# Optimization experiments

Measured on AMD Instinct MI355X. Metric: run time of the kernel, lower is better.

## Reference

```python
import jax, jax.numpy as jnp
import numpy as np

NEG_SLOPE = 0.2


def _add_self_loops(edge_index, n_nodes):
    loop = jnp.arange(n_nodes, dtype=edge_index.dtype)
    src = jnp.concatenate([edge_index[0], loop])
    dst = jnp.concatenate([edge_index[1], loop])
    return src, dst


def _gat_layer(x, src, dst, W, a_src, a_dst, b):
    # PyG GATConv, heads=1: h = x @ W; e_ij = LeakyReLU(a_src.h_j + a_dst.h_i)
    # softmax over incoming edges of each dst node, then weighted aggregate.
    n = x.shape[0]
    h = x @ W                      # [N, d]
    s = h @ a_src                  # [N] per-source score
    t = h @ a_dst                  # [N] per-dest score
    e = jax.nn.leaky_relu(s[src] + t[dst], NEG_SLOPE)          # [E]
    m = jax.ops.segment_max(e, dst, num_segments=n)            # stable softmax
    ex = jnp.exp(e - m[dst])
    denom = jax.ops.segment_sum(ex, dst, num_segments=n)
    alpha = ex / denom[dst]                                     # [E]
    out = jax.ops.segment_sum(h[src] * alpha[:, None], dst, num_segments=n)
    return out + b


def setup_inputs() -> dict:
    key = jax.random.key(0)
    ks = jax.random.split(key, 16)
    N, E, d = 50000, 800000, 64
    sc = 1.0 / np.sqrt(d)
    inp = {
        "x": jax.random.normal(ks[0], (N, d), dtype=jnp.float32),
        "edge_index": jax.random.randint(ks[1], (2, E), 0, N, dtype=jnp.int64),
    }
    for i, layer in enumerate((1, 2, 3)):
        inp[f"W{layer}"] = jax.random.normal(ks[2 + 4 * i], (d, d), dtype=jnp.float32) * sc
        inp[f"a_src{layer}"] = jax.random.normal(ks[3 + 4 * i], (d,), dtype=jnp.float32) * sc
        inp[f"a_dst{layer}"] = jax.random.normal(ks[4 + 4 * i], (d,), dtype=jnp.float32) * sc
        inp[f"b{layer}"] = jnp.zeros((d,), dtype=jnp.float32)
    return inp


def reference(x, edge_index, W1, a_src1, a_dst1, b1, W2, a_src2, a_dst2, b2,
              W3, a_src3, a_dst3, b3):
    n = x.shape[0]
    src, dst = _add_self_loops(edge_index, n)
    x = jax.nn.relu(_gat_layer(x, src, dst, W1, a_src1, a_dst1, b1))
    x = jax.nn.relu(_gat_layer(x, src, dst, W2, a_src2, a_dst2, b2))
    x = jax.nn.relu(_gat_layer(x, src, dst, W3, a_src3, a_dst3, b3))
    return x
```

## Files before the change

kernel.cpp:

```cpp
#include <hip/hip_runtime.h>
#include <hip/hip_fp16.h>

#define NEG_SLOPE 0.2f
#define MAXDEG 64

__device__ __forceinline__ float readlane_f(float v, int l) {
    return __uint_as_float(__builtin_amdgcn_readlane(__float_as_uint(v), l));
}
__device__ __forceinline__ int readlane_i(int v, int l) {
    return __builtin_amdgcn_readlane(v, l);
}


__device__ __forceinline__ void bucket_body(const int* __restrict__ ei, int E,
                                            int* __restrict__ cnt, int* __restrict__ slots,
                                            int bid) {
    int t = bid * 256 + threadIdx.x;
    int base = t * 8;
    if (base >= E) return;
    int s[8], d[8];
    if (base + 7 < E) {
        int4 sa = *(const int4*)(ei + base);
        int4 sb = *(const int4*)(ei + base + 4);
        int4 da = *(const int4*)(ei + E + base);
        int4 db = *(const int4*)(ei + E + base + 4);
        s[0]=sa.x; s[1]=sa.y; s[2]=sa.z; s[3]=sa.w; s[4]=sb.x; s[5]=sb.y; s[6]=sb.z; s[7]=sb.w;
        d[0]=da.x; d[1]=da.y; d[2]=da.z; d[3]=da.w; d[4]=db.x; d[5]=db.y; d[6]=db.z; d[7]=db.w;
    } else {
        #pragma unroll
        for (int j = 0; j < 8; j++) {
            int e = base + j;
            if (e < E) { s[j] = ei[e]; d[j] = ei[E + e]; }
            else       { s[j] = -1;    d[j] = -1; }
        }
    }
    int pos[8];
    #pragma unroll
    for (int j = 0; j < 8; j++)
        pos[j] = (d[j] >= 0) ? atomicAdd(&cnt[d[j]], 1) : MAXDEG;
    #pragma unroll
    for (int j = 0; j < 8; j++)
        if (pos[j] < MAXDEG)
            __builtin_nontemporal_store(s[j], &slots[(size_t)d[j] * MAXDEG + pos[j]]);
}


__device__ __forceinline__ void gemm_body(const float* __restrict__ x, const float* __restrict__ W,
                                          const float* __restrict__ a_src, const float* __restrict__ a_dst,
                                          __half* __restrict__ h16, float* __restrict__ sv,
                                          float* __restrict__ tv, int n, int bid) {
    __shared__ float Wl[64 * 64];
    __shared__ float Xl[64 * 68];
    int tid = threadIdx.x;
    int n0 = bid * 64;

    #pragma unroll
    for (int r = 0; r < 4; r++) {
        int f = tid + r * 256;
        int k = f >> 4, c = (f & 15) * 4;
        *(float4*)(&Wl[k * 64 + c]) = *(const float4*)(W + (size_t)f * 4);
    }
    #pragma unroll
    for (int r = 0; r < 4; r++) {
        int f = tid + r * 256;
        int node = f >> 4, k = (f & 15) * 4;
        float4 xv = make_float4(0.f, 0.f, 0.f, 0.f);
        if (n0 + node < n) xv = *(const float4*)(x + (size_t)(n0 + node) * 64 + k);
        Xl[(k + 0) * 68 + node] = xv.x;
        Xl[(k + 1) * 68 + node] = xv.y;
        Xl[(k + 2) * 68 + node] = xv.z;
        Xl[(k + 3) * 68 + node] = xv.w;
    }
    __syncthreads();

    int tx = tid & 15, ty = tid >> 4;
    float acc[4][4] = {{0.f}};
    #pragma unroll 16
    for (int k = 0; k < 64; k++) {
        float4 xv = *(const float4*)(&Xl[k * 68 + ty * 4]);
        float4 wv = *(const float4*)(&Wl[k * 64 + tx * 4]);
        acc[0][0] += xv.x * wv.x; acc[0][1] += xv.x * wv.y; acc[0][2] += xv.x * wv.z; acc[0][3] += xv.x * wv.w;
        acc[1][0] += xv.y * wv.x; acc[1][1] += xv.y * wv.y; acc[1][2] += xv.y * wv.z; acc[1][3] += xv.y * wv.w;
        acc[2][0] += xv.z * wv.x; acc[2][1] += xv.z * wv.y; acc[2][2] += xv.z * wv.z; acc[2][3] += xv.z * wv.w;
        acc[3][0] += xv.w * wv.x; acc[3][1] += xv.w * wv.y; acc[3][2] += xv.w * wv.z; acc[3][3] += xv.w * wv.w;
    }

    float4 as4 = *(const float4*)(a_src + tx * 4);
    float4 ad4 = *(const float4*)(a_dst + tx * 4);
    #pragma unroll
    for (int j = 0; j < 4; j++) {
        int node = n0 + ty * 4 + j;
        float sp = acc[j][0] * as4.x + acc[j][1] * as4.y + acc[j][2] * as4.z + acc[j][3] * as4.w;
        float tp = acc[j][0] * ad4.x + acc[j][1] * ad4.y + acc[j][2] * ad4.z + acc[j][3] * ad4.w;
        #pragma unroll
        for (int o = 1; o < 16; o <<= 1) {
            sp += __shfl_xor(sp, o);
            tp += __shfl_xor(tp, o);
        }
        if (node < n) {
            union { __half2 h2[2]; uint2 u; } pk;
            pk.h2[0] = __floats2half2_rn(acc[j][0], acc[j][1]);
            pk.h2[1] = __floats2half2_rn(acc[j][2], acc[j][3]);
            *(uint2*)(h16 + (size_t)node * 64 + tx * 4) = pk.u;
            if (tx == 0) { sv[node] = sp; tv[node] = tp; }
        }
    }
}

__global__ __launch_bounds__(256) void k_fused1(const int* __restrict__ ei, int E,
                                                int* __restrict__ cnt, int* __restrict__ slots,
                                                const float* __restrict__ x, const float* __restrict__ W,
                                                const float* __restrict__ a_src, const float* __restrict__ a_dst,
                                                __half* __restrict__ h16, float* __restrict__ sv,
                                                float* __restrict__ tv, int n, int gB) {
    int bid = blockIdx.x;
    if (bid < gB) bucket_body(ei, E, cnt, slots, bid);
    else          gemm_body(x, W, a_src, a_dst, h16, sv, tv, n, bid - gB);
}

__global__ __launch_bounds__(256) void k_gemm(const float* __restrict__ x, const float* __restrict__ W,
                                              const float* __restrict__ a_src, const float* __restrict__ a_dst,
                                              __half* __restrict__ h16, float* __restrict__ sv,
                                              float* __restrict__ tv, int n) {
    gemm_body(x, W, a_src, a_dst, h16, sv, tv, n, blockIdx.x);
}


#define GATHER8(K)                                                            \
    {                                                                         \
        float e0 = readlane_f(ex, (K) + 0), e1 = readlane_f(ex, (K) + 1);     \
        float e2 = readlane_f(ex, (K) + 2), e3 = readlane_f(ex, (K) + 3);     \
        float e4 = readlane_f(ex, (K) + 4), e5 = readlane_f(ex, (K) + 5);     \
        float e6 = readlane_f(ex, (K) + 6), e7 = readlane_f(ex, (K) + 7);     \
        int s0 = readlane_i(sid, (K) + 0), s1 = readlane_i(sid, (K) + 1);     \
        int s2 = readlane_i(sid, (K) + 2), s3 = readlane_i(sid, (K) + 3);     \
        int s4 = readlane_i(sid, (K) + 4), s5 = readlane_i(sid, (K) + 5);     \
        int s6 = readlane_i(sid, (K) + 6), s7 = readlane_i(sid, (K) + 7);     \
        float v0 = __half2float(h16[(size_t)s0 * 64 + lane]);                 \
        float v1 = __half2float(h16[(size_t)s1 * 64 + lane]);                 \
        float v2 = __half2float(h16[(size_t)s2 * 64 + lane]);                 \
        float v3 = __half2float(h16[(size_t)s3 * 64 + lane]);                 \
        float v4 = __half2float(h16[(size_t)s4 * 64 + lane]);                 \
        float v5 = __half2float(h16[(size_t)s5 * 64 + lane]);                 \
        float v6 = __half2float(h16[(size_t)s6 * 64 + lane]);                 \
        float v7 = __half2float(h16[(size_t)s7 * 64 + lane]);                 \
        acc0 += e0 * v0; acc1 += e1 * v1; acc2 += e2 * v2; acc3 += e3 * v3;   \
        acc0 += e4 * v4; acc1 += e5 * v5; acc2 += e6 * v6; acc3 += e7 * v7;   \
    }

__global__ __launch_bounds__(1024) void k_agg(const __half* __restrict__ h16, const float* __restrict__ sv,
                                              const float* __restrict__ tv, const int* __restrict__ cnt,
                                              const int* __restrict__ slots, const float* __restrict__ bias,
                                              float* __restrict__ xout, int n) {
    int wid = (blockIdx.x * 1024 + threadIdx.x) >> 6;
    int lane = threadIdx.x & 63;
    if (wid >= n) return;
    int deg = cnt[wid];
    if (deg > 63) deg = 63;
    int ecount = deg + 1;
    float tn = tv[wid];

    int sid = 0;
    bool valid = lane < ecount;
    if (valid) sid = (lane == deg) ? wid : slots[(size_t)wid * MAXDEG + lane];
    float ss = valid ? sv[sid] : 0.f;
    float ev = ss + tn;
    ev = (ev > 0.f) ? ev : NEG_SLOPE * ev;
    float ex = valid ? __expf(ev) : 0.f;

    float denom = ex;
    #pragma unroll
    for (int o = 1; o < 64; o <<= 1) denom += __shfl_xor(denom, o);

    float acc0 = 0.f, acc1 = 0.f, acc2 = 0.f, acc3 = 0.f;
    if (ecount <= 24) {
        GATHER8(0) GATHER8(8) GATHER8(16)
    } else {
        int cnt8 = (ecount + 7) & ~7;
        for (int k = 0; k < cnt8; k += 8) GATHER8(k)
    }

    float o = (acc0 + acc1) + (acc2 + acc3);
    o = o / denom + bias[lane];
    xout[(size_t)wid * 64 + lane] = fmaxf(o, 0.f);
}


extern "C" void kernel_launch(void* const* d_in, const int* in_sizes, int n_in,
                              void* d_out, int out_size, void* d_ws, size_t ws_size,
                              hipStream_t stream) {
    const float* x0 = (const float*)d_in[0];
    const int* ei = (const int*)d_in[1];
    const float* Wp[3]    = {(const float*)d_in[2],  (const float*)d_in[6],  (const float*)d_in[10]};
    const float* asp[3]   = {(const float*)d_in[3],  (const float*)d_in[7],  (const float*)d_in[11]};
    const float* adp[3]   = {(const float*)d_in[4],  (const float*)d_in[8],  (const float*)d_in[12]};
    const float* bp[3]    = {(const float*)d_in[5],  (const float*)d_in[9],  (const float*)d_in[13]};

    int N = in_sizes[0] / 64;
    int E = in_sizes[1] / 2;

    size_t nf = (size_t)N * 64;
    float* bufA = (float*)d_ws;
    float* sArr = bufA + nf;
    float* tArr = sArr + N;
    int* cntArr = (int*)(tArr + N);
    int* slots  = cntArr + N;
    __half* h16 = (__half*)(slots + (size_t)N * MAXDEG);

    hipMemsetAsync(cntArr, 0, (size_t)N * sizeof(int), stream);

    int gB = ((E + 7) / 8 + 255) / 256;
    int gG = (N + 63) / 64;
    int gAgg = (N + 15) / 16;

    k_fused1<<<gB + gG, 256, 0, stream>>>(ei, E, cntArr, slots,
                                          x0, Wp[0], asp[0], adp[0], h16, sArr, tArr, N, gB);
    k_agg<<<gAgg, 1024, 0, stream>>>(h16, sArr, tArr, cntArr, slots, bp[0], bufA, N);
    k_gemm<<<gG, 256, 0, stream>>>(bufA, Wp[1], asp[1], adp[1], h16, sArr, tArr, N);
    k_agg<<<gAgg, 1024, 0, stream>>>(h16, sArr, tArr, cntArr, slots, bp[1], bufA, N);
    k_gemm<<<gG, 256, 0, stream>>>(bufA, Wp[2], asp[2], adp[2], h16, sArr, tArr, N);
    k_agg<<<gAgg, 1024, 0, stream>>>(h16, sArr, tArr, cntArr, slots, bp[2], (float*)d_out, N);
}
```

Before: 181.7 us.

## Fuse aggregation with next layer's GEMM via shared-memory tile

Adds a k_fusedA kernel in which each 256-thread block aggregates 64 destination nodes (16 per wave) and writes the ReLU'd results into shared memory. It then runs the next layer's 64x64 GEMM and attention-score dots on that tile directly, double-buffering h16/s/t across layers. This removes the fp32 intermediate round trip through global memory and two kernel launches. In exchange, the aggregation runs with fewer threads per block and the blocks process their nodes serially, which may lower the parallelism available to hide gather latency.

```diff
diff --git a/kernel.cpp b/kernel.cpp
--- a/kernel.cpp
+++ b/kernel.cpp
@@ -45,34 +45,11 @@
 }
 
 
-__device__ __forceinline__ void gemm_body(const float* __restrict__ x, const float* __restrict__ W,
-                                          const float* __restrict__ a_src, const float* __restrict__ a_dst,
-                                          __half* __restrict__ h16, float* __restrict__ sv,
-                                          float* __restrict__ tv, int n, int bid) {
-    __shared__ float Wl[64 * 64];
-    __shared__ float Xl[64 * 68];
+__device__ __forceinline__ void gemm_compute(const float* __restrict__ Wl, const float* __restrict__ Xl,
+                                             const float* __restrict__ a_src, const float* __restrict__ a_dst,
+                                             __half* __restrict__ h16, float* __restrict__ sv,
+                                             float* __restrict__ tv, int n, int n0) {
     int tid = threadIdx.x;
-    int n0 = bid * 64;
-
-    #pragma unroll
-    for (int r = 0; r < 4; r++) {
-        int f = tid + r * 256;
-        int k = f >> 4, c = (f & 15) * 4;
-        *(float4*)(&Wl[k * 64 + c]) = *(const float4*)(W + (size_t)f * 4);
-    }
-    #pragma unroll
-    for (int r = 0; r < 4; r++) {
-        int f = tid + r * 256;
-        int node = f >> 4, k = (f & 15) * 4;
-        float4 xv = make_float4(0.f, 0.f, 0.f, 0.f);
-        if (n0 + node < n) xv = *(const float4*)(x + (size_t)(n0 + node) * 64 + k);
-        Xl[(k + 0) * 68 + node] = xv.x;
-        Xl[(k + 1) * 68 + node] = xv.y;
-        Xl[(k + 2) * 68 + node] = xv.z;
-        Xl[(k + 3) * 68 + node] = xv.w;
-    }
-    __syncthreads();
-
     int tx = tid & 15, ty = tid >> 4;
     float acc[4][4] = {{0.f}};
     #pragma unroll 16
@@ -84,7 +61,6 @@
         acc[2][0] += xv.z * wv.x; acc[2][1] += xv.z * wv.y; acc[2][2] += xv.z * wv.z; acc[2][3] += xv.z * wv.w;
         acc[3][0] += xv.w * wv.x; acc[3][1] += xv.w * wv.y; acc[3][2] += xv.w * wv.z; acc[3][3] += xv.w * wv.w;
     }
-
     float4 as4 = *(const float4*)(a_src + tx * 4);
     float4 ad4 = *(const float4*)(a_dst + tx * 4);
     #pragma unroll
@@ -107,6 +83,36 @@
     }
 }
 
+
+__device__ __forceinline__ void gemm_body(const float* __restrict__ x, const float* __restrict__ W,
+                                          const float* __restrict__ a_src, const float* __restrict__ a_dst,
+                                          __half* __restrict__ h16, float* __restrict__ sv,
+                                          float* __restrict__ tv, int n, int bid) {
+    __shared__ float Wl[64 * 64];
+    __shared__ float Xl[64 * 68];
+    int tid = threadIdx.x;
+    int n0 = bid * 64;
+    #pragma unroll
+    for (int r = 0; r < 4; r++) {
+        int f = tid + r * 256;
+        int k = f >> 4, c = (f & 15) * 4;
+        *(float4*)(&Wl[k * 64 + c]) = *(const float4*)(W + (size_t)f * 4);
+    }
+    #pragma unroll
+    for (int r = 0; r < 4; r++) {
+        int f = tid + r * 256;
+        int node = f >> 4, k = (f & 15) * 4;
+        float4 xv = make_float4(0.f, 0.f, 0.f, 0.f);
+        if (n0 + node < n) xv = *(const float4*)(x + (size_t)(n0 + node) * 64 + k);
+        Xl[(k + 0) * 68 + node] = xv.x;
+        Xl[(k + 1) * 68 + node] = xv.y;
+        Xl[(k + 2) * 68 + node] = xv.z;
+        Xl[(k + 3) * 68 + node] = xv.w;
+    }
+    __syncthreads();
+    gemm_compute(Wl, Xl, a_src, a_dst, h16, sv, tv, n, n0);
+}
+
 __global__ __launch_bounds__(256) void k_fused1(const int* __restrict__ ei, int E,
                                                 int* __restrict__ cnt, int* __restrict__ slots,
                                                 const float* __restrict__ x, const float* __restrict__ W,
@@ -118,15 +124,8 @@
     else          gemm_body(x, W, a_src, a_dst, h16, sv, tv, n, bid - gB);
 }
 
-__global__ __launch_bounds__(256) void k_gemm(const float* __restrict__ x, const float* __restrict__ W,
-                                              const float* __restrict__ a_src, const float* __restrict__ a_dst,
-                                              __half* __restrict__ h16, float* __restrict__ sv,
-                                              float* __restrict__ tv, int n) {
-    gemm_body(x, W, a_src, a_dst, h16, sv, tv, n, blockIdx.x);
-}
-
-
-#define GATHER8(K)                                                            \
+
+#define GATHER8(H, K)                                                         \
     {                                                                         \
         float e0 = readlane_f(ex, (K) + 0), e1 = readlane_f(ex, (K) + 1);     \
         float e2 = readlane_f(ex, (K) + 2), e3 = readlane_f(ex, (K) + 3);     \
@@ -136,17 +135,75 @@
         int s2 = readlane_i(sid, (K) + 2), s3 = readlane_i(sid, (K) + 3);     \
         int s4 = readlane_i(sid, (K) + 4), s5 = readlane_i(sid, (K) + 5);     \
         int s6 = readlane_i(sid, (K) + 6), s7 = readlane_i(sid, (K) + 7);     \
-        float v0 = __half2float(h16[(size_t)s0 * 64 + lane]);                 \
-        float v1 = __half2float(h16[(size_t)s1 * 64 + lane]);                 \
-        float v2 = __half2float(h16[(size_t)s2 * 64 + lane]);                 \
-        float v3 = __half2float(h16[(size_t)s3 * 64 + lane]);                 \
-        float v4 = __half2float(h16[(size_t)s4 * 64 + lane]);                 \
-        float v5 = __half2float(h16[(size_t)s5 * 64 + lane]);                 \
-        float v6 = __half2float(h16[(size_t)s6 * 64 + lane]);                 \
-        float v7 = __half2float(h16[(size_t)s7 * 64 + lane]);                 \
+        float v0 = __half2float(H[(size_t)s0 * 64 + lane]);                   \
+        float v1 = __half2float(H[(size_t)s1 * 64 + lane]);                   \
+        float v2 = __half2float(H[(size_t)s2 * 64 + lane]);                   \
+        float v3 = __half2float(H[(size_t)s3 * 64 + lane]);                   \
+        float v4 = __half2float(H[(size_t)s4 * 64 + lane]);                   \
+        float v5 = __half2float(H[(size_t)s5 * 64 + lane]);                   \
+        float v6 = __half2float(H[(size_t)s6 * 64 + lane]);                   \
+        float v7 = __half2float(H[(size_t)s7 * 64 + lane]);                   \
         acc0 += e0 * v0; acc1 += e1 * v1; acc2 += e2 * v2; acc3 += e3 * v3;   \
         acc0 += e4 * v4; acc1 += e5 * v5; acc2 += e6 * v6; acc3 += e7 * v7;   \
     }
+
+__device__ __forceinline__ float agg_node(const __half* __restrict__ h16, const float* __restrict__ sv,
+                                          const float* __restrict__ tv, const int* __restrict__ cnt,
+                                          const int* __restrict__ slots, int node, int lane) {
+    int deg = cnt[node];
+    if (deg > 63) deg = 63;
+    int ecount = deg + 1;
+    float tn = tv[node];
+    int sid = 0;
+    bool valid = lane < ecount;
+    if (valid) sid = (lane == deg) ? node : slots[(size_t)node * MAXDEG + lane];
+    float ss = valid ? sv[sid] : 0.f;
+    float ev = ss + tn;
+    ev = (ev > 0.f) ? ev : NEG_SLOPE * ev;
+    float ex = valid ? __expf(ev) : 0.f;
+    float denom = ex;
+    #pragma unroll
+    for (int o = 1; o < 64; o <<= 1) denom += __shfl_xor(denom, o);
+    float acc0 = 0.f, acc1 = 0.f, acc2 = 0.f, acc3 = 0.f;
+    if (ecount <= 24) {
+        GATHER8(h16, 0) GATHER8(h16, 8) GATHER8(h16, 16)
+    } else {
+        int cnt8 = (ecount + 7) & ~7;
+        for (int k = 0; k < cnt8; k += 8) GATHER8(h16, k)
+    }
+    return ((acc0 + acc1) + (acc2 + acc3)) / denom;
+}
+
+
+__global__ __launch_bounds__(256) void k_fusedA(const __half* __restrict__ h16in, const float* __restrict__ svin,
+                                                const float* __restrict__ tvin, const int* __restrict__ cnt,
+                                                const int* __restrict__ slots, const float* __restrict__ bias,
+                                                const float* __restrict__ W, const float* __restrict__ a_src,
+                                                const float* __restrict__ a_dst, __half* __restrict__ h16out,
+                                                float* __restrict__ svout, float* __restrict__ tvout, int n) {
+    __shared__ float Wl[64 * 64];
+    __shared__ float Xl[64 * 68];
+    int tid = threadIdx.x;
+    int n0 = blockIdx.x * 64;
+    #pragma unroll
+    for (int r = 0; r < 4; r++) {
+        int f = tid + r * 256;
+        *(float4*)(&Wl[(f >> 4) * 64 + (f & 15) * 4]) = *(const float4*)(W + (size_t)f * 4);
+    }
+    int lane = tid & 63;
+    int w = tid >> 6;
+    float bl = bias[lane];
+    for (int i = 0; i < 16; i++) {
+        int node = n0 + w * 16 + i;
+        if (node >= n) break;
+        float o = agg_node(h16in, svin, tvin, cnt, slots, node, lane);
+        o = fmaxf(o + bl, 0.f);
+        Xl[lane * 68 + (node - n0)] = o;
+    }
+    __syncthreads();
+    gemm_compute(Wl, Xl, a_src, a_dst, h16out, svout, tvout, n, n0);
+}
+
 
 __global__ __launch_bounds__(1024) void k_agg(const __half* __restrict__ h16, const float* __restrict__ sv,
                                               const float* __restrict__ tv, const int* __restrict__ cnt,
@@ -155,33 +212,8 @@
     int wid = (blockIdx.x * 1024 + threadIdx.x) >> 6;
     int lane = threadIdx.x & 63;
     if (wid >= n) return;
-    int deg = cnt[wid];
-    if (deg > 63) deg = 63;
-    int ecount = deg + 1;
-    float tn = tv[wid];
-
-    int sid = 0;
-    bool valid = lane < ecount;
-    if (valid) sid = (lane == deg) ? wid : slots[(size_t)wid * MAXDEG + lane];
-    float ss = valid ? sv[sid] : 0.f;
-    float ev = ss + tn;
-    ev = (ev > 0.f) ? ev : NEG_SLOPE * ev;
-    float ex = valid ? __expf(ev) : 0.f;
-
-    float denom = ex;
-    #pragma unroll
-    for (int o = 1; o < 64; o <<= 1) denom += __shfl_xor(denom, o);
-
-    float acc0 = 0.f, acc1 = 0.f, acc2 = 0.f, acc3 = 0.f;
-    if (ecount <= 24) {
-        GATHER8(0) GATHER8(8) GATHER8(16)
-    } else {
-        int cnt8 = (ecount + 7) & ~7;
-        for (int k = 0; k < cnt8; k += 8) GATHER8(k)
-    }
-
-    float o = (acc0 + acc1) + (acc2 + acc3);
-    o = o / denom + bias[lane];
+    float o = agg_node(h16, sv, tv, cnt, slots, wid, lane);
+    o = o + bias[lane];
     xout[(size_t)wid * 64 + lane] = fmaxf(o, 0.f);
 }
 
@@ -199,13 +231,14 @@
     int N = in_sizes[0] / 64;
     int E = in_sizes[1] / 2;
 
-    size_t nf = (size_t)N * 64;
-    float* bufA = (float*)d_ws;
-    float* sArr = bufA + nf;
-    float* tArr = sArr + N;
-    int* cntArr = (int*)(tArr + N);
+    float* svA  = (float*)d_ws;
+    float* tvA  = svA + N;
+    float* svB  = tvA + N;
+    float* tvB  = svB + N;
+    int* cntArr = (int*)(tvB + N);
     int* slots  = cntArr + N;
-    __half* h16 = (__half*)(slots + (size_t)N * MAXDEG);
+    __half* h16A = (__half*)(slots + (size_t)N * MAXDEG);
+    __half* h16B = h16A + (size_t)N * 64;
 
     hipMemsetAsync(cntArr, 0, (size_t)N * sizeof(int), stream);
 
@@ -214,10 +247,10 @@
     int gAgg = (N + 15) / 16;
 
     k_fused1<<<gB + gG, 256, 0, stream>>>(ei, E, cntArr, slots,
-                                          x0, Wp[0], asp[0], adp[0], h16, sArr, tArr, N, gB);
-    k_agg<<<gAgg, 1024, 0, stream>>>(h16, sArr, tArr, cntArr, slots, bp[0], bufA, N);
-    k_gemm<<<gG, 256, 0, stream>>>(bufA, Wp[1], asp[1], adp[1], h16, sArr, tArr, N);
-    k_agg<<<gAgg, 1024, 0, stream>>>(h16, sArr, tArr, cntArr, slots, bp[1], bufA, N);
-    k_gemm<<<gG, 256, 0, stream>>>(bufA, Wp[2], asp[2], adp[2], h16, sArr, tArr, N);
-    k_agg<<<gAgg, 1024, 0, stream>>>(h16, sArr, tArr, cntArr, slots, bp[2], (float*)d_out, N);
-}
+                                          x0, Wp[0], asp[0], adp[0], h16A, svA, tvA, N, gB);
+    k_fusedA<<<gG, 256, 0, stream>>>(h16A, svA, tvA, cntArr, slots, bp[0],
+                                     Wp[1], asp[1], adp[1], h16B, svB, tvB, N);
+    k_fusedA<<<gG, 256, 0, stream>>>(h16B, svB, tvB, cntArr, slots, bp[1],
+                                     Wp[2], asp[2], adp[2], h16A, svA, tvA, N);
+    k_agg<<<gAgg, 1024, 0, stream>>>(h16A, svA, tvA, cntArr, slots, bp[2], (float*)d_out, N);
+}
```

Result: no change. 184.9 us (+1.8%).
